# Performance work log

Measured on AMD Instinct MI355X. Metric: run time of the kernel, lower is better.

Reference implementation:

```python
import jax, jax.numpy as jnp
import numpy as np

K_ACT = 5          # k_active regimes
TAU = 0.5          # resample temperature
N = 8192           # n_particles (scaled to production size)
DZ, DM, KT, DE = 32, 64, 15, 16  # d_latent, d_mamba, k_regimes+10, d_regime_embed


def _lin(x, W, b):
    # torch nn.Linear convention: y = x @ W.T + b
    return x @ W.T + b


def setup_inputs() -> dict:
    key = jax.random.key(0)
    ks = iter(jax.random.split(key, 48))

    def rn(shape, s=1.0):
        return jax.random.normal(next(ks), shape, jnp.float32) * s

    inp = dict(
        remaining_high=jax.random.uniform(next(ks), (N,), jnp.float32) * 5.0 + 1.0,
        remaining_low=jax.random.uniform(next(ks), (N,), jnp.float32) * 5.0 + 1.0,
        z=rn((N, DZ)),
        regime_logits=rn((N, KT)),
        log_weights=rn((N,), 0.5),
        h_t=rn((DM,)),
        obs_remaining=jnp.float32(3.0),
        eps_high=rn((N,)),
        eps_low=rn((N,)),
        u_gumbel=jax.random.uniform(next(ks), (N, N), jnp.float32),
        embed=rn((KT, DE), 0.1),
        W_rt1=rn((32, DM + DE), 0.1), b_rt1=jnp.zeros(32, jnp.float32),
        W_rt2=rn((KT, 32), 0.1), b_rt2=jnp.zeros(KT, jnp.float32),
        W_d1=rn((64, DM + DE + DZ), 0.1), b_d1=jnp.zeros(64, jnp.float32),
        W_d2=rn((32, 64), 0.1), b_d2=jnp.zeros(32, jnp.float32),
        W_d3=rn((4, 32), 0.1), b_d3=jnp.zeros(4, jnp.float32),
        W_g=rn((DZ, DM + DE + DZ), 0.1), b_g=jnp.zeros(DZ, jnp.float32),
        W_c=rn((DZ, DM + DE + DZ), 0.1), b_c=jnp.zeros(DZ, jnp.float32),
        log_R=jnp.array([np.log(0.5), np.log(0.4), np.log(0.6)], jnp.float32),
        log_obs_scale=rn((KT,), 0.1),
        W_a1=rn((16, DM), 0.1), b_a1=jnp.zeros(16, jnp.float32),
        W_a2=rn((1, 16), 0.1), b_a2=jnp.zeros(1, jnp.float32),
    )
    return inp


def reference(remaining_high, remaining_low, z, regime_logits, log_weights, h_t,
              obs_remaining, eps_high, eps_low, u_gumbel, embed,
              W_rt1, b_rt1, W_rt2, b_rt2, W_d1, b_d1, W_d2, b_d2, W_d3, b_d3,
              W_g, b_g, W_c, b_c, log_R, log_obs_scale, W_a1, b_a1, W_a2, b_a2):
    silu = jax.nn.silu
    n = remaining_high.shape[0]
    h = jnp.broadcast_to(h_t, (n, h_t.shape[0]))  # (N, d_mamba)

    # ---- transition (predict step) ----
    rp = jax.nn.softmax(regime_logits, axis=-1)[:, :K_ACT]          # (N, K)
    remb = rp @ embed[:K_ACT]                                        # (N, d_embed)
    ri = jnp.concatenate([h, remb], axis=-1)                         # (N, 80)
    upd = _lin(silu(_lin(ri, W_rt1, b_rt1)), W_rt2, b_rt2)[:, :K_ACT]
    new_logits = regime_logits.at[:, :K_ACT].set(
        0.7 * regime_logits[:, :K_ACT] + 0.3 * upd)
    di = jnp.concatenate([h, remb, z], axis=-1)                      # (N, 112)
    dp = _lin(silu(_lin(silu(_lin(di, W_d1, b_d1)), W_d2, b_d2)), W_d3, b_d3)
    sig_h = jax.nn.softplus(dp[:, 2]) + 0.01
    sig_l = jax.nn.softplus(dp[:, 3]) + 0.01
    nh = jnp.clip(remaining_high + dp[:, 0] + sig_h * eps_high, 0.0)
    nl = jnp.clip(remaining_low + dp[:, 1] + sig_l * eps_low, 0.0)
    gate = jax.nn.sigmoid(_lin(di, W_g, b_g))
    nz = gate * z + (1.0 - gate) * jnp.tanh(_lin(di, W_c, b_c))

    # ---- observation: skew-normal log-likelihood (source_idx=0, 'high') ----
    R_src = jnp.clip(jnp.exp(log_R[0]), 0.15, 2.5)
    alpha = _lin(silu(_lin(h_t[None, :], W_a1, b_a1)), W_a2, b_a2)[0, 0]
    scales = jax.nn.softplus(log_obs_scale[:K_ACT])
    nrp = jax.nn.softmax(new_logits, axis=-1)[:, :K_ACT]
    R = jnp.clip(R_src * (nrp @ scales), 0.15, 4.0)                  # (N,)
    zz = (obs_remaining - nh) / R
    loglik = (jnp.log(2.0) - jnp.log(R) - 0.5 * jnp.log(2.0 * jnp.pi)
              - 0.5 * zz * zz + jax.scipy.stats.norm.logcdf(alpha * zz))

    # ---- weight update + normalization ----
    lw = log_weights + loglik
    lw = lw - jax.scipy.special.logsumexp(lw)

    # ---- soft resample (Gumbel-softmax relaxation) ----
    g = -jnp.log(-jnp.log(u_gumbel + 1e-10) + 1e-10)                 # (N, N)
    sa = jax.nn.softmax((lw[None, :] + g) / TAU, axis=-1)            # (N, N)
    state = jnp.concatenate([nh[:, None], nl[:, None], nz, new_logits], axis=-1)  # (N, 49)
    return sa @ state  # resampled [high | low | z | regime_logits]
```

## Files before the change

kernel.cpp:

```cpp
#include <hip/hip_runtime.h>
#include <math.h>

#define NP 8192

using f32x4  = __attribute__((ext_vector_type(4))) float;
using bf16x8 = __attribute__((ext_vector_type(8))) short;

__device__ __forceinline__ unsigned short f2bf(float x) {
  unsigned int u = __float_as_uint(x);
  u = (u + 0x7FFFu + ((u >> 16) & 1u)) >> 16;
  return (unsigned short)u;
}
__device__ __forceinline__ float fast_log2(float x) { float r; asm("v_log_f32 %0, %1" : "=v"(r) : "v"(x)); return r; }
__device__ __forceinline__ float fast_exp2(float x) { float r; asm("v_exp_f32 %0, %1" : "=v"(r) : "v"(x)); return r; }
__device__ __forceinline__ float siluf(float x) { return x / (1.0f + expf(-x)); }
__device__ __forceinline__ float softplusf(float x) { return (x > 20.0f) ? x : log1pf(expf(x)); }
__device__ __forceinline__ float dot4(const float4 a, const float4 b) {
  return a.x * b.x + a.y * b.y + a.z * b.z + a.w * b.w;
}


__global__ __launch_bounds__(128) void k_particle(
    const float* __restrict__ rh,   const float* __restrict__ rlo,
    const float* __restrict__ z,    const float* __restrict__ rlog,
    const float* __restrict__ logw, const float* __restrict__ h_t,
    const float* __restrict__ obs_p,
    const float* __restrict__ eps_h, const float* __restrict__ eps_l,
    const float* __restrict__ embed,
    const float* __restrict__ W_rt1, const float* __restrict__ b_rt1,
    const float* __restrict__ W_rt2, const float* __restrict__ b_rt2,
    const float* __restrict__ W_d1,  const float* __restrict__ b_d1,
    const float* __restrict__ W_d2,  const float* __restrict__ b_d2,
    const float* __restrict__ W_d3,  const float* __restrict__ b_d3,
    const float* __restrict__ W_g,   const float* __restrict__ b_g,
    const float* __restrict__ W_c,   const float* __restrict__ b_c,
    const float* __restrict__ log_R, const float* __restrict__ log_obs_scale,
    const float* __restrict__ W_a1,  const float* __restrict__ b_a1,
    const float* __restrict__ W_a2,  const float* __restrict__ b_a2,
    float* __restrict__ a_out, unsigned short* __restrict__ Bt) {
  __shared__ float d1c[64 * 48];
  __shared__ float gcs[32 * 48];
  __shared__ float ccs[32 * 48];
  __shared__ float rt1c[32 * 16];
  __shared__ float d2s[32 * 64];
  __shared__ float d3s[4 * 32];
  __shared__ float rt2s[5 * 32];
  __shared__ float embs[80];
  __shared__ float cD1[64], cRT1[32], cG[32], cC[32];
  __shared__ float bD2[32], bD3[4], bRT2[8];
  __shared__ float a1s[16], scal[8];
  __shared__ float x1ex[32 * 68];
  __shared__ float tx[32 * 36];
  __shared__ float stex[32 * 52];

  const int t = threadIdx.x;

#define STAGEM(DST, SRC, ROWS, SSTR, C0, NC)                          \
  for (int e = t; e < (ROWS) * (NC); e += 128) {                      \
    const int ro = e / (NC);                                          \
    const int co = e - ro * (NC);                                     \
    DST[e] = SRC[ro * (SSTR) + (C0) + co];                            \
  }
  STAGEM(d1c, W_d1, 64, 112, 64, 48)
  STAGEM(gcs, W_g, 32, 112, 64, 48)
  STAGEM(ccs, W_c, 32, 112, 64, 48)
  STAGEM(rt1c, W_rt1, 32, 80, 64, 16)
#undef STAGEM
  for (int e = t; e < 2048; e += 128) d2s[e] = W_d2[e];
  if (t < 128) d3s[t] = W_d3[t];
  for (int e = t; e < 160; e += 128) rt2s[e] = W_rt2[e];
  if (t < 80) embs[t] = embed[t];
  if (t < 32) bD2[t] = b_d2[t];
  if (t < 4)  bD3[t] = b_d3[t];
  if (t < 5)  bRT2[t] = b_rt2[t];

  for (int o = t; o < 160; o += 128) {
    const float* wr; float bb;
    if (o < 64)       { wr = W_d1 + o * 112;        bb = b_d1[o]; }
    else if (o < 96)  { wr = W_rt1 + (o - 64) * 80; bb = b_rt1[o - 64]; }
    else if (o < 128) { wr = W_g + (o - 96) * 112;  bb = b_g[o - 96]; }
    else              { wr = W_c + (o - 128) * 112; bb = b_c[o - 128]; }
    float acc = bb;
    #pragma unroll
    for (int m = 0; m < 64; m += 4)
      acc += dot4(*(const float4*)(wr + m), *(const float4*)(h_t + m));
    if (o < 64) cD1[o] = acc;
    else if (o < 96) cRT1[o - 64] = acc;
    else if (o < 128) cG[o - 96] = acc;
    else cC[o - 128] = acc;
  }
  if (t < 16) {
    float acc = b_a1[t];
    #pragma unroll
    for (int m = 0; m < 64; m += 4)
      acc += dot4(*(const float4*)(W_a1 + t * 64 + m), *(const float4*)(h_t + m));
    a1s[t] = siluf(acc);
  } else if (t == 16) {
    scal[1] = fminf(fmaxf(expf(log_R[0]), 0.15f), 2.5f);
  } else if (t >= 17 && t < 22) {
    scal[2 + t - 17] = softplusf(log_obs_scale[t - 17]);
  }
  __syncthreads();
  if (t == 0) {
    float acc = b_a2[0];
    #pragma unroll
    for (int k = 0; k < 16; ++k) acc += W_a2[k] * a1s[k];
    scal[0] = acc;
  }

  const int l = t & 63, lbase = l & ~3;
  const int q = t >> 2, s = t & 3;
  const int j = blockIdx.x * 32 + q;
  const float obs = obs_p[0];

  float rlj[15];
  #pragma unroll
  for (int k = 0; k < 15; ++k) rlj[k] = rlog[j * 15 + k];
  float m0 = rlj[0];
  #pragma unroll
  for (int k = 1; k < 15; ++k) m0 = fmaxf(m0, rlj[k]);
  float sum = 0.0f, e5[5];
  #pragma unroll
  for (int k = 0; k < 15; ++k) { float e = expf(rlj[k] - m0); if (k < 5) e5[k] = e; sum += e; }
  const float inv = 1.0f / sum;

  float remb[16];
  #pragma unroll
  for (int c = 0; c < 16; ++c) {
    float acc = e5[0] * embs[c];
    #pragma unroll
    for (int k = 1; k < 5; ++k) acc += e5[k] * embs[k * 16 + c];
    remb[c] = acc * inv;
  }

  float zj[32];
  #pragma unroll
  for (int c = 0; c < 32; c += 4) {
    const float4 v = *(const float4*)(z + j * 32 + c);
    zj[c] = v.x; zj[c + 1] = v.y; zj[c + 2] = v.z; zj[c + 3] = v.w;
  }

  #pragma unroll
  for (int r = 0; r < 8; ++r) {
    const int o = 4 * r + s;
    float acc = cRT1[o];
    #pragma unroll
    for (int c = 0; c < 16; ++c) acc += rt1c[o * 16 + c] * remb[c];
    tx[q * 36 + o] = siluf(acc);
  }
  __syncthreads();
  float t1[32];
  #pragma unroll
  for (int c = 0; c < 32; c += 4) {
    const float4 v = *(const float4*)(tx + q * 36 + c);
    t1[c] = v.x; t1[c + 1] = v.y; t1[c + 2] = v.z; t1[c + 3] = v.w;
  }
  float updS = bRT2[s], upd4 = bRT2[4];
  #pragma unroll
  for (int c = 0; c < 32; ++c) { updS += rt2s[s * 32 + c] * t1[c]; upd4 += rt2s[128 + c] * t1[c]; }
  float nlg[15];
  #pragma unroll
  for (int k = 0; k < 4; ++k) nlg[k] = 0.7f * rlj[k] + 0.3f * __shfl(updS, lbase + k);
  nlg[4] = 0.7f * rlj[4] + 0.3f * upd4;
  #pragma unroll
  for (int k = 5; k < 15; ++k) nlg[k] = rlj[k];

  #pragma unroll
  for (int r = 0; r < 16; ++r) {
    const int o = 4 * r + s;
    const float* wrow = d1c + o * 48;
    float acc = cD1[o];
    #pragma unroll
    for (int c = 0; c < 16; ++c) acc += wrow[c] * remb[c];
    #pragma unroll
    for (int c = 0; c < 32; ++c) acc += wrow[16 + c] * zj[c];
    x1ex[q * 68 + o] = siluf(acc);
  }
  __syncthreads();

  float acc8[8];
  #pragma unroll
  for (int r = 0; r < 8; ++r) acc8[r] = bD2[4 * r + s];
  #pragma unroll
  for (int half = 0; half < 2; ++half) {
    float xh[32];
    #pragma unroll
    for (int c = 0; c < 32; c += 4) {
      const float4 v = *(const float4*)(x1ex + q * 68 + half * 32 + c);
      xh[c] = v.x; xh[c + 1] = v.y; xh[c + 2] = v.z; xh[c + 3] = v.w;
    }
    #pragma unroll
    for (int r = 0; r < 8; ++r) {
      const int o = 4 * r + s;
      #pragma unroll
      for (int c = 0; c < 32; ++c) acc8[r] += d2s[o * 64 + half * 32 + c] * xh[c];
    }
  }
  #pragma unroll
  for (int r = 0; r < 8; ++r) tx[q * 36 + 4 * r + s] = siluf(acc8[r]);
  __syncthreads();
  float x2v[32];
  #pragma unroll
  for (int c = 0; c < 32; c += 4) {
    const float4 v = *(const float4*)(tx + q * 36 + c);
    x2v[c] = v.x; x2v[c + 1] = v.y; x2v[c + 2] = v.z; x2v[c + 3] = v.w;
  }
  float dps = bD3[s];
  #pragma unroll
  for (int c = 0; c < 32; ++c) dps += d3s[s * 32 + c] * x2v[c];
  const float dp0 = __shfl(dps, lbase), dp1 = __shfl(dps, lbase + 1);
  const float dp2 = __shfl(dps, lbase + 2), dp3 = __shfl(dps, lbase + 3);
  const float sig_h = softplusf(dp2) + 0.01f;
  const float sig_l = softplusf(dp3) + 0.01f;
  const float nh = fmaxf(rh[j] + dp0 + sig_h * eps_h[j], 0.0f);
  const float nl = fmaxf(rlo[j] + dp1 + sig_l * eps_l[j], 0.0f);

  #pragma unroll
  for (int r = 0; r < 8; ++r) {
    const int o = 4 * r + s;
    const float* gr = gcs + o * 48;
    const float* cr = ccs + o * 48;
    float ga = cG[o], caa = cC[o];
    #pragma unroll
    for (int c = 0; c < 16; ++c) { ga += gr[c] * remb[c]; caa += cr[c] * remb[c]; }
    #pragma unroll
    for (int c = 0; c < 32; ++c) { ga += gr[16 + c] * zj[c]; caa += cr[16 + c] * zj[c]; }
    const float gs = 1.0f / (1.0f + expf(-ga));
    stex[q * 52 + 2 + o] = gs * zj[o] + (1.0f - gs) * tanhf(caa);
  }

  if (s == 0) {
    stex[q * 52 + 0] = nh;
    stex[q * 52 + 1] = nl;
    #pragma unroll
    for (int k = 0; k < 15; ++k) stex[q * 52 + 34 + k] = nlg[k];
    float m1 = nlg[0];
    #pragma unroll
    for (int k = 1; k < 15; ++k) m1 = fmaxf(m1, nlg[k]);
    float sum1 = 0.0f, e5b[5];
    #pragma unroll
    for (int k = 0; k < 15; ++k) { float e = expf(nlg[k] - m1); if (k < 5) e5b[k] = e; sum1 += e; }
    float dot = 0.0f;
    #pragma unroll
    for (int k = 0; k < 5; ++k) dot += e5b[k] * scal[2 + k];
    dot /= sum1;
    const float R  = fminf(fmaxf(scal[1] * dot, 0.15f), 4.0f);
    const float zz = (obs - nh) / R;
    const float xx = scal[0] * zz;
    float lcdf;
    if (xx > -6.0f) {
      double p = 0.5 * erfc(-(double)xx * 0.7071067811865475244);
      lcdf = (float)log(p);
    } else {
      const float ix2 = 1.0f / (xx * xx);
      const float ser = 1.0f + ix2 * (-1.0f + ix2 * (3.0f + ix2 * (-15.0f + ix2 * 105.0f)));
      lcdf = -0.5f * xx * xx - logf(-xx) - 0.918938533f + logf(ser);
    }
    const float loglik = 0.693147181f - logf(R) - 0.918938533f - 0.5f * zz * zz + lcdf;
    a_out[j] = (logw[j] + loglik) * 2.8853900817779268f;
  }
  __syncthreads();

  if (t < 64) {
    const int c = t;
    const int b = c >> 4, rowc = c & 15;
    if (c < 49) {
      #pragma unroll
      for (int m = 0; m < 4; ++m) {
        bf16x8 v8;
        #pragma unroll
        for (int r = 0; r < 8; ++r) v8[r] = (short)f2bf(stex[(8 * m + r) * 52 + c]);
        *(bf16x8*)(Bt + (size_t)(((blockIdx.x * 4 + b) * 64) + m * 16 + rowc) * 8) = v8;
      }
    } else if (c == 49) {
      bf16x8 v8;
      #pragma unroll
      for (int r = 0; r < 8; ++r) v8[r] = (short)0x3F80;
      #pragma unroll
      for (int m = 0; m < 4; ++m)
        *(bf16x8*)(Bt + (size_t)(((blockIdx.x * 4 + b) * 64) + m * 16 + rowc) * 8) = v8;
    } else {
      bf16x8 v8;
      #pragma unroll
      for (int r = 0; r < 8; ++r) v8[r] = 0;
      #pragma unroll
      for (int m = 0; m < 4; ++m)
        *(bf16x8*)(Bt + (size_t)(((blockIdx.x * 4 + b) * 64) + m * 16 + rowc) * 8) = v8;
    }
  }
}

#define WSTR 1032
__global__ __launch_bounds__(512) void k_resample(const float* __restrict__ u,
                                                  const float* __restrict__ a,
                                                  const unsigned short* __restrict__ Bt,
                                                  float* __restrict__ out) {
  __shared__ unsigned short Wlds[16 * WSTR];
  __shared__ float cacc[8][64][16];
  __shared__ float zrow[16];
  const int t = threadIdx.x;
  const int w = t >> 6, l = t & 63;
  const int i0 = blockIdx.x << 4;

  f32x4 acc0 = {0.f, 0.f, 0.f, 0.f}, acc1 = acc0, acc2 = acc0, acc3 = acc0;

  for (int chunk = 0; chunk < 8; ++chunk) {
    const int c0 = chunk << 10;
    #pragma unroll
    for (int p = 0; p < 4; ++p) {
      const int fidx = (p << 12) + (t << 3);
      const int rr = fidx >> 10, col = fidx & 1023;
      const float* up = u + (size_t)(i0 + rr) * NP + c0 + col;
      const float4 ua = *(const float4*)(up);
      const float4 ub = *(const float4*)(up + 4);
      const float4 aa = *(const float4*)(a + c0 + col);
      const float4 ab = *(const float4*)(a + c0 + col + 4);
      const float uu[8] = {ua.x, ua.y, ua.z, ua.w, ub.x, ub.y, ub.z, ub.w};
      const float av[8] = {aa.x, aa.y, aa.z, aa.w, ab.x, ab.y, ab.z, ab.w};
      bf16x8 wv8;
      #pragma unroll
      for (int e = 0; e < 8; ++e) {
        const float t1 = fast_log2(uu[e] + 1e-10f);
        const float t2 = fmaf(t1, -0.69314718056f, 1e-10f);
        const float t3 = fast_log2(t2);
        const float wv = fast_exp2(fmaf(t3, -2.0f, av[e]));
        wv8[e] = (short)f2bf(wv);
      }
      *(bf16x8*)(&Wlds[rr * WSTR + col]) = wv8;
    }
    __syncthreads();
    #pragma unroll
    for (int it = 0; it < 4; ++it) {
      const int kb   = (w << 2) + it;
      const int jblk = (c0 >> 5) + kb;
      const bf16x8 af = *(const bf16x8*)(&Wlds[(l & 15) * WSTR + (kb << 5) + ((l >> 4) << 3)]);
      const unsigned short* bp = Bt + (size_t)(jblk << 2) * 512;
      const bf16x8 b0 = *(const bf16x8*)(bp + (0 * 64 + l) * 8);
      const bf16x8 b1 = *(const bf16x8*)(bp + (1 * 64 + l) * 8);
      const bf16x8 b2 = *(const bf16x8*)(bp + (2 * 64 + l) * 8);
      const bf16x8 b3 = *(const bf16x8*)(bp + (3 * 64 + l) * 8);
      acc0 = __builtin_amdgcn_mfma_f32_16x16x32_bf16(af, b0, acc0, 0, 0, 0);
      acc1 = __builtin_amdgcn_mfma_f32_16x16x32_bf16(af, b1, acc1, 0, 0, 0);
      acc2 = __builtin_amdgcn_mfma_f32_16x16x32_bf16(af, b2, acc2, 0, 0, 0);
      acc3 = __builtin_amdgcn_mfma_f32_16x16x32_bf16(af, b3, acc3, 0, 0, 0);
    }
    __syncthreads();
  }

  #pragma unroll
  for (int r = 0; r < 4; ++r) {
    cacc[w][l][0 * 4 + r] = acc0[r];
    cacc[w][l][1 * 4 + r] = acc1[r];
    cacc[w][l][2 * 4 + r] = acc2[r];
    cacc[w][l][3 * 4 + r] = acc3[r];
  }
  __syncthreads();

  const int c = t & 63;
  float v[2];
  #pragma unroll
  for (int rr = 0; rr < 2; ++rr) {
    const int r    = ((t >> 6) << 1) + rr;
    const int lsrc = ((r >> 2) << 4) | (c & 15);
    const int reg  = ((c >> 4) << 2) + (r & 3);
    float sv = 0.0f;
    #pragma unroll
    for (int ww = 0; ww < 8; ++ww) sv += cacc[ww][lsrc][reg];
    v[rr] = sv;
    if (c == 49) zrow[r] = sv;
  }
  __syncthreads();
  if (c < 49) {
    #pragma unroll
    for (int rr = 0; rr < 2; ++rr) {
      const int r = ((t >> 6) << 1) + rr;
      out[(size_t)(i0 + r) * 49 + c] = v[rr] / zrow[r];
    }
  }
}

extern "C" void kernel_launch(void* const* d_in, const int* in_sizes, int n_in,
                              void* d_out, int out_size, void* d_ws, size_t ws_size,
                              hipStream_t stream) {
  const float* rh    = (const float*)d_in[0];
  const float* rlo   = (const float*)d_in[1];
  const float* z     = (const float*)d_in[2];
  const float* rlog  = (const float*)d_in[3];
  const float* logw  = (const float*)d_in[4];
  const float* h_t   = (const float*)d_in[5];
  const float* obs   = (const float*)d_in[6];
  const float* eps_h = (const float*)d_in[7];
  const float* eps_l = (const float*)d_in[8];
  const float* u     = (const float*)d_in[9];
  const float* embed = (const float*)d_in[10];
  const float* W_rt1 = (const float*)d_in[11];
  const float* b_rt1 = (const float*)d_in[12];
  const float* W_rt2 = (const float*)d_in[13];
  const float* b_rt2 = (const float*)d_in[14];
  const float* W_d1  = (const float*)d_in[15];
  const float* b_d1  = (const float*)d_in[16];
  const float* W_d2  = (const float*)d_in[17];
  const float* b_d2  = (const float*)d_in[18];
  const float* W_d3  = (const float*)d_in[19];
  const float* b_d3  = (const float*)d_in[20];
  const float* W_g   = (const float*)d_in[21];
  const float* b_g   = (const float*)d_in[22];
  const float* W_c   = (const float*)d_in[23];
  const float* b_c   = (const float*)d_in[24];
  const float* log_R = (const float*)d_in[25];
  const float* log_obs_scale = (const float*)d_in[26];
  const float* W_a1  = (const float*)d_in[27];
  const float* b_a1  = (const float*)d_in[28];
  const float* W_a2  = (const float*)d_in[29];
  const float* b_a2  = (const float*)d_in[30];

  float* ws_a = (float*)((char*)d_ws + 36864);
  unsigned short* ws_bt = (unsigned short*)((char*)d_ws + 73728);

  k_particle<<<256, 128, 0, stream>>>(rh, rlo, z, rlog, logw, h_t, obs, eps_h, eps_l,
                                      embed, W_rt1, b_rt1, W_rt2, b_rt2,
                                      W_d1, b_d1, W_d2, b_d2, W_d3, b_d3,
                                      W_g, b_g, W_c, b_c, log_R, log_obs_scale,
                                      W_a1, b_a1, W_a2, b_a2, ws_a, ws_bt);
  k_resample<<<512, 512, 0, stream>>>(u, ws_a, ws_bt, (float*)d_out);
}
```

Before: 468.9 us.

## Give each wave a private column range to drop block barriers in resample

The resample kernel used to stage all 16 rows × 1024 columns of Gumbel weights into shared LDS per chunk, with two block-wide barriers per chunk. Now each wave owns a contiguous 1024-column slice of the particle dimension. It loads u in 128-column groups, writes its own private LDS tile, and feeds its MFMAs directly, with no __syncthreads inside the loop. This removes 16 block barriers and lets waves run independently. In exchange, the per-lane loads shrink to float4 with row-strided access, and correctness relies on wave-internal ordering of the LDS write and read.

```diff
diff --git a/kernel.cpp b/kernel.cpp
--- a/kernel.cpp
+++ b/kernel.cpp
@@ -4,6 +4,7 @@
 #define NP 8192
 
 using f32x4  = __attribute__((ext_vector_type(4))) float;
+using bf16x4 = __attribute__((ext_vector_type(4))) short;
 using bf16x8 = __attribute__((ext_vector_type(8))) short;
 
 __device__ __forceinline__ unsigned short f2bf(float x) {
@@ -290,50 +291,51 @@
   }
 }
 
-#define WSTR 1032
+#define RSTR 136
 __global__ __launch_bounds__(512) void k_resample(const float* __restrict__ u,
                                                   const float* __restrict__ a,
                                                   const unsigned short* __restrict__ Bt,
                                                   float* __restrict__ out) {
-  __shared__ unsigned short Wlds[16 * WSTR];
+  __shared__ unsigned short Wlds[8][16][RSTR];
   __shared__ float cacc[8][64][16];
   __shared__ float zrow[16];
   const int t = threadIdx.x;
   const int w = t >> 6, l = t & 63;
   const int i0 = blockIdx.x << 4;
+  const int jw = w << 10;
+  const int lc = (l & 31) << 2;
+  const int rh2 = l >> 5;
 
   f32x4 acc0 = {0.f, 0.f, 0.f, 0.f}, acc1 = acc0, acc2 = acc0, acc3 = acc0;
 
-  for (int chunk = 0; chunk < 8; ++chunk) {
-    const int c0 = chunk << 10;
-    #pragma unroll
-    for (int p = 0; p < 4; ++p) {
-      const int fidx = (p << 12) + (t << 3);
-      const int rr = fidx >> 10, col = fidx & 1023;
-      const float* up = u + (size_t)(i0 + rr) * NP + c0 + col;
-      const float4 ua = *(const float4*)(up);
-      const float4 ub = *(const float4*)(up + 4);
-      const float4 aa = *(const float4*)(a + c0 + col);
-      const float4 ab = *(const float4*)(a + c0 + col + 4);
-      const float uu[8] = {ua.x, ua.y, ua.z, ua.w, ub.x, ub.y, ub.z, ub.w};
-      const float av[8] = {aa.x, aa.y, aa.z, aa.w, ab.x, ab.y, ab.z, ab.w};
-      bf16x8 wv8;
-      #pragma unroll
-      for (int e = 0; e < 8; ++e) {
-        const float t1 = fast_log2(uu[e] + 1e-10f);
+  for (int g = 0; g < 8; ++g) {
+    const int cb = jw + (g << 7);
+    const float4 av = *(const float4*)(a + cb + lc);
+    float4 uv[8];
+    #pragma unroll
+    for (int q2 = 0; q2 < 8; ++q2) {
+      const int row = (q2 << 1) + rh2;
+      uv[q2] = *(const float4*)(u + (size_t)(i0 + row) * NP + cb + lc);
+    }
+    #pragma unroll
+    for (int q2 = 0; q2 < 8; ++q2) {
+      const int row = (q2 << 1) + rh2;
+      bf16x4 wv4;
+      #pragma unroll
+      for (int e = 0; e < 4; ++e) {
+        const float ue = (e == 0) ? uv[q2].x : (e == 1) ? uv[q2].y : (e == 2) ? uv[q2].z : uv[q2].w;
+        const float ae = (e == 0) ? av.x : (e == 1) ? av.y : (e == 2) ? av.z : av.w;
+        const float t1 = fast_log2(ue + 1e-10f);
         const float t2 = fmaf(t1, -0.69314718056f, 1e-10f);
         const float t3 = fast_log2(t2);
-        const float wv = fast_exp2(fmaf(t3, -2.0f, av[e]));
-        wv8[e] = (short)f2bf(wv);
+        wv4[e] = (short)f2bf(fast_exp2(fmaf(t3, -2.0f, ae)));
       }
-      *(bf16x8*)(&Wlds[rr * WSTR + col]) = wv8;
-    }
-    __syncthreads();
-    #pragma unroll
-    for (int it = 0; it < 4; ++it) {
-      const int kb   = (w << 2) + it;
-      const int jblk = (c0 >> 5) + kb;
-      const bf16x8 af = *(const bf16x8*)(&Wlds[(l & 15) * WSTR + (kb << 5) + ((l >> 4) << 3)]);
+      *(bf16x4*)(&Wlds[w][row][lc]) = wv4;
+    }
+    #pragma unroll
+    for (int kbl = 0; kbl < 4; ++kbl) {
+      const int jblk = (cb >> 5) + kbl;
+      const bf16x8 af = *(const bf16x8*)(&Wlds[w][l & 15][(kbl << 5) + ((l >> 4) << 3)]);
       const unsigned short* bp = Bt + (size_t)(jblk << 2) * 512;
       const bf16x8 b0 = *(const bf16x8*)(bp + (0 * 64 + l) * 8);
       const bf16x8 b1 = *(const bf16x8*)(bp + (1 * 64 + l) * 8);
@@ -344,9 +346,9 @@
       acc2 = __builtin_amdgcn_mfma_f32_16x16x32_bf16(af, b2, acc2, 0, 0, 0);
       acc3 = __builtin_amdgcn_mfma_f32_16x16x32_bf16(af, b3, acc3, 0, 0, 0);
     }
-    __syncthreads();
-  }
-
+  }
+
+  __syncthreads();
   #pragma unroll
   for (int r = 0; r < 4; ++r) {
     cacc[w][l][0 * 4 + r] = acc0[r];
```

Measured after the change: 470.6 us. About the same (+0.4%).
